# Optimization experiments

Measured on AMD Instinct MI355X. Metric: run time of the kernel, lower is better.

Reference implementation:

```python
import jax, jax.numpy as jnp
import numpy as np

# Problem constants (from init_kwargs)
NUM_NODES = 120000
NUM_MOVABLE = 100000
NUM_NETS = 100000
NUM_PINS = 400000
NBX = 256
NBY = 256
XL, XH, YL, YH = 0.0, 1000.0, 0.0, 1000.0
BSX = (XH - XL) / NBX  # bin_size_x
BSY = (YH - YL) / NBY  # bin_size_y
UNIT_H_CAP = 1.5  # unit_horizontal_routing_capacity
UNIT_V_CAP = 1.5  # unit_vertical_routing_capacity
MAX_RATE = 2.0    # max_route_opt_adjust_rate
MIN_RATE = 1.0 / MAX_RATE
EPS = 1e-6


def setup_inputs() -> dict:
    key = jax.random.key(0)
    k1, k2, k3, k4, k5, k6, k7, k8 = jax.random.split(key, 8)
    pos = jnp.concatenate([
        jax.random.uniform(k1, (NUM_NODES,), jnp.float32, XL, XH - 10.0),
        jax.random.uniform(k2, (NUM_NODES,), jnp.float32, YL, YH - 10.0)])
    pin_pos = jnp.concatenate([
        jax.random.uniform(k3, (NUM_PINS,), jnp.float32, XL, XH),
        jax.random.uniform(k4, (NUM_PINS,), jnp.float32, YL, YH)])
    node_size_x = jax.random.uniform(k5, (NUM_NODES,), jnp.float32, 1.0, 8.0)
    node_size_y = jax.random.uniform(k6, (NUM_NODES,), jnp.float32, 1.0, 4.0)
    flat_netpin = jax.random.randint(k7, (NUM_PINS,), 0, NUM_PINS, jnp.int32)
    inner = jnp.sort(jax.random.randint(k8, (NUM_NETS - 1,), 0, NUM_PINS, jnp.int32))
    netpin_start = jnp.concatenate([
        jnp.zeros((1,), jnp.int32), inner, jnp.full((1,), NUM_PINS, jnp.int32)])
    return dict(pos=pos, pin_pos=pin_pos, node_size_x=node_size_x,
                node_size_y=node_size_y, netpin_start=netpin_start,
                flat_netpin=flat_netpin)


def _bin_overlap(lo, hi, origin, bin_size, nbins):
    # lo, hi: [K] interval per item; returns [K, nbins] overlap length with each bin
    edges = origin + jnp.arange(nbins, dtype=lo.dtype) * bin_size  # [nbins]
    return jnp.clip(jnp.minimum(hi[:, None], edges + bin_size)
                    - jnp.maximum(lo[:, None], edges), 0.0)


def reference(pos, pin_pos, node_size_x, node_size_y, netpin_start, flat_netpin):
    num_pins = flat_netpin.shape[0]
    # --- per-net bounding boxes from ragged netpin lists (CSR) ---
    slot = jnp.arange(num_pins, dtype=jnp.int32)
    net_id = jnp.clip(jnp.searchsorted(netpin_start, slot, side='right') - 1,
                      0, NUM_NETS - 1)
    px = pin_pos[flat_netpin]
    py = pin_pos[num_pins + flat_netpin]
    xmin = jax.ops.segment_min(px, net_id, NUM_NETS, indices_are_sorted=True)
    xmax = jax.ops.segment_max(px, net_id, NUM_NETS, indices_are_sorted=True)
    ymin = jax.ops.segment_min(py, net_id, NUM_NETS, indices_are_sorted=True)
    ymax = jax.ops.segment_max(py, net_id, NUM_NETS, indices_are_sorted=True)
    valid = (xmax >= xmin) & (ymax >= ymin)  # nets with >=1 pin
    span_x = jnp.where(valid, xmax - xmin, 0.0)
    span_y = jnp.where(valid, ymax - ymin, 0.0)
    # RUDY demand density: horizontal demand per unit area = 1/span_y, etc.
    coef_h = jnp.where(valid & (span_y > EPS), 1.0 / jnp.maximum(span_y, EPS), 0.0)
    coef_v = jnp.where(valid & (span_x > EPS), 1.0 / jnp.maximum(span_x, EPS), 0.0)
    xmin_c = jnp.where(valid, xmin, XL)
    xmax_c = jnp.where(valid, xmax, XL)
    ymin_c = jnp.where(valid, ymin, YL)
    ymax_c = jnp.where(valid, ymax, YL)
    # separable bin overlaps: [N, NBX], [N, NBY]
    ox = _bin_overlap(xmin_c, xmax_c, XL, BSX, NBX)
    oy = _bin_overlap(ymin_c, ymax_c, YL, BSY, NBY)
    # scatter demand into 2D bin grid (rank-1 per net, summed via einsum)
    H = jnp.einsum('nx,ny->xy', ox * coef_h[:, None], oy)
    V = jnp.einsum('nx,ny->xy', ox * coef_v[:, None], oy)
    # capacity adjustment + clamp
    bin_area = BSX * BSY
    util = jnp.maximum(H / (bin_area * UNIT_H_CAP), V / (bin_area * UNIT_V_CAP))
    util = jnp.clip(util, MIN_RATE, MAX_RATE)
    # --- gather bin utilization back per movable node ---
    nxl = pos[:NUM_MOVABLE]
    nyl = pos[NUM_NODES:NUM_NODES + NUM_MOVABLE]
    nxh = nxl + node_size_x[:NUM_MOVABLE]
    nyh = nyl + node_size_y[:NUM_MOVABLE]
    nox = _bin_overlap(nxl, nxh, XL, BSX, NBX)  # [M, NBX]
    noy = _bin_overlap(nyl, nyh, YL, BSY, NBY)  # [M, NBY]
    instance_route_area = jnp.einsum('mx,xy,my->m', nox, util, noy)
    return instance_route_area
```

## Files before the change

kernel.cpp:

```cpp
#include <hip/hip_runtime.h>

#define NUM_NODES   120000
#define NUM_MOVABLE 100000
#define NUM_NETS    100000
#define NUM_PINS    400000
#define NBX 256
#define NBY 256
#define GRID_BINS (NBX*NBY)
#define SC_BLOCKS 32
#define SEGCAP 192

constexpr float BSX      = 1000.0f / 256.0f;
constexpr float INV_BS   = 256.0f / 1000.0f;
constexpr float BIN_AREA = BSX * BSX;
constexpr float EPSV     = 1e-6f;


__global__ void pin_bbox(const float* __restrict__ pin_pos,
                         const int* __restrict__ netpin_start,
                         const int* __restrict__ flat_netpin,
                         float4* __restrict__ bbox) {
    __shared__ int snp[260];
    __shared__ int sbound[2];
    int B0 = blockIdx.x * 256;
    int t  = B0 + threadIdx.x;
    if (threadIdx.x < 2) {
        int q = (threadIdx.x == 0) ? B0 : min(B0 + 255, NUM_PINS - 1);
        int lo = 0, hi = NUM_NETS + 1;
        while (lo < hi) {
            int mid = (lo + hi) >> 1;
            if (netpin_start[mid] <= q) lo = mid + 1; else hi = mid;
        }
        sbound[threadIdx.x] = min(lo - 1, NUM_NETS - 1);
    }
    __syncthreads();
    int netlo = sbound[0];
    int cnt   = sbound[1] - netlo + 2;
    for (int i = threadIdx.x; i < cnt; i += 256) snp[i] = netpin_start[netlo + i];
    __syncthreads();

    int key = -4;
    int net = -1, segend = -1;
    float xmn = 3.4e38f, xmx = -3.4e38f, ymn = 3.4e38f, ymx = -3.4e38f;
    if (t < NUM_PINS) {
        int lo = 0, hi = cnt;
        while (lo < hi) {
            int mid = (lo + hi) >> 1;
            if (snp[mid] <= t) lo = mid + 1; else hi = mid;
        }
        int li = lo - 1;
        net    = netlo + li;
        segend = snp[li + 1];
        key    = (net << 1) | (snp[li] == t ? 1 : 0);
        int p = flat_netpin[t];
        float px = pin_pos[p];
        float py = pin_pos[NUM_PINS + p];
        xmn = px; xmx = px; ymn = py; ymx = py;
    }
    int lane = threadIdx.x & 63;
    for (int d = 1; d < 64; d <<= 1) {
        int   ku = __shfl_up(key, d);
        float a  = __shfl_up(xmn, d);
        float b  = __shfl_up(xmx, d);
        float c  = __shfl_up(ymn, d);
        float e  = __shfl_up(ymx, d);
        if (lane >= d && (ku >> 1) == (key >> 1)) {
            xmn = fminf(xmn, a); xmx = fmaxf(xmx, b);
            ymn = fminf(ymn, c); ymx = fmaxf(ymx, e);
            key |= (ku & 1);
        }
    }
    int nextkey = __shfl_down(key, 1);
    if (t >= NUM_PINS || net < 0) return;
    bool netchg = (lane == 63) ? false : ((nextkey >> 1) != (key >> 1));
    bool tail   = (lane == 63) || netchg;
    if (!tail) return;
    bool true_end  = netchg || (segend == t + 1);
    bool contained = (key & 1) != 0;
    if (contained && true_end) {
        bbox[net] = make_float4(xmn, ymn, xmx, ymx);
    } else {
        unsigned* bp = (unsigned*)(bbox + net);
        atomicMin(bp + 0, __float_as_uint(xmn));
        atomicMin(bp + 1, __float_as_uint(ymn));
        atomicMax((int*)bp + 2, (int)__float_as_uint(xmx));
        atomicMax((int*)bp + 3, (int)__float_as_uint(ymx));
    }
}

__global__ __launch_bounds__(1024) void scatter_nets(
        const float4* __restrict__ bbox,
        unsigned* __restrict__ cnt_rb,
        unsigned* __restrict__ entries) {
    __shared__ unsigned cur[256];
    int t = threadIdx.x, blk = blockIdx.x;
    if (t < 256) cur[t] = 0u;
    __syncthreads();
    int start = blk * 4096;
    #pragma unroll
    for (int k = 0; k < 4; ++k) {
        int n = start + k * 1024 + t;
        if (n < NUM_NETS) {
            float4 b = bbox[n];
            if ((b.w - b.y) > EPSV || (b.z - b.x) > EPSV) {
                unsigned bxl = (unsigned)min((int)(b.x * INV_BS), NBX - 1);
                unsigned bxh = (unsigned)min((int)(b.z * INV_BS), NBX - 1);
                unsigned p0 = atomicAdd(&cur[bxl], 1u);
                if (p0 < SEGCAP)
                    entries[(bxl * 32 + blk) * SEGCAP + p0] = (unsigned)(n << 1);
                unsigned p1 = atomicAdd(&cur[bxh], 1u);
                if (p1 < SEGCAP)
                    entries[(bxh * 32 + blk) * SEGCAP + p1] = (unsigned)(n << 1) | 1u;
            }
        }
    }
    __syncthreads();
    if (t < 256) cnt_rb[t * 32 + blk] = min(cur[t], (unsigned)SEGCAP);
}

__global__ __launch_bounds__(1024) void splat_rows(
        const float4* __restrict__ bbox,
        const unsigned* __restrict__ cnt_rb,
        const unsigned* __restrict__ entries,
        float* __restrict__ A_hT, float* __restrict__ B_hT,
        float* __restrict__ A_vT, float* __restrict__ B_vT) {
    int bx = blockIdx.x;
    int t  = threadIdx.x;
    __shared__ float F[8][NBY];
    __shared__ unsigned pref[33];
    for (int i = t; i < 8 * NBY; i += 1024) ((float*)F)[i] = 0.0f;
    if (t == 0) {
        unsigned run = 0;
        for (int s = 0; s < 32; ++s) { pref[s] = run; run += cnt_rb[bx * 32 + s]; }
        pref[32] = run;
    }
    __syncthreads();
    int total = (int)pref[32];

    for (int j = t; j < total; j += 1024) {
        int lo = 0, hi = 32;
        while (lo + 1 < hi) {
            int mid = (lo + hi) >> 1;
            if ((int)pref[mid] <= j) lo = mid; else hi = mid;
        }
        unsigned e = entries[(bx * 32 + lo) * SEGCAP + (j - (int)pref[lo])];
        int n = (int)(e >> 1), side = (int)(e & 1u);
        float4 b = bbox[n];
        float span_x = b.z - b.x, span_y = b.w - b.y;
        float coef_h = (span_y > EPSV) ? 1.0f / span_y : 0.0f;
        float coef_v = (span_x > EPSV) ? 1.0f / span_x : 0.0f;
        int byl = min((int)(b.y * INV_BS), NBY - 1);
        int byh = min((int)(b.w * INV_BS), NBY - 1);
        float ryl = (float)(byl + 1) * BSX - b.y;
        float ryh = (float)(byh + 1) * BSX - b.w;
        float rx, s0;
        if (side == 0) {
            int bxl = min((int)(b.x * INV_BS), NBX - 1);
            rx = (float)(bxl + 1) * BSX - b.x; s0 = 1.0f;
        } else {
            int bxh = min((int)(b.z * INV_BS), NBX - 1);
            rx = (float)(bxh + 1) * BSX - b.z; s0 = -1.0f;
        }
        if (coef_h != 0.0f) {
            float w0 = s0 * coef_h, w1 = -s0 * coef_h;
            atomicAdd(&F[0][byl], w0 * rx  * ryl);
            atomicAdd(&F[1][byl], w0 * rx  * BSX);
            atomicAdd(&F[2][byl], w0 * BSX * ryl);
            atomicAdd(&F[3][byl], w0 * BSX * BSX);
            atomicAdd(&F[0][byh], w1 * rx  * ryh);
            atomicAdd(&F[1][byh], w1 * rx  * BSX);
            atomicAdd(&F[2][byh], w1 * BSX * ryh);
            atomicAdd(&F[3][byh], w1 * BSX * BSX);
        }
        if (coef_v != 0.0f) {
            float w0 = s0 * coef_v, w1 = -s0 * coef_v;
            atomicAdd(&F[4][byl], w0 * rx  * ryl);
            atomicAdd(&F[5][byl], w0 * rx  * BSX);
            atomicAdd(&F[6][byl], w0 * BSX * ryl);
            atomicAdd(&F[7][byl], w0 * BSX * BSX);
            atomicAdd(&F[4][byh], w1 * rx  * ryh);
            atomicAdd(&F[5][byh], w1 * rx  * BSX);
            atomicAdd(&F[6][byh], w1 * BSX * ryh);
            atomicAdd(&F[7][byh], w1 * BSX * BSX);
        }
    }
    __syncthreads();

    int g = t >> 8, y = t & 255;
    float* f = F[2 * g + 1];
    for (int d = 1; d < 256; d <<= 1) {
        float add = (y >= d) ? f[y - d] : 0.0f;
        __syncthreads();
        f[y] += add;
        __syncthreads();
    }
    float ex  = (y > 0) ? F[2 * g + 1][y - 1] : 0.0f;
    float val = F[2 * g][y] + ex;
    float* o  = (g == 0) ? A_hT : (g == 1) ? B_hT : (g == 2) ? A_vT : B_vT;
    o[y * NBX + bx] = val;
}

__global__ void scan_x_util(const float* __restrict__ A_hT, const float* __restrict__ B_hT,
                            const float* __restrict__ A_vT, const float* __restrict__ B_vT,
                            float* __restrict__ util) {
    int y = blockIdx.x, x = threadIdx.x;
    int idxT = y * NBX + x;
    __shared__ float2 tmp[NBX];
    tmp[x] = make_float2(B_hT[idxT], B_vT[idxT]);
    __syncthreads();
    for (int d = 1; d < 256; d <<= 1) {
        float2 add = (x >= d) ? tmp[x - d] : make_float2(0.f, 0.f);
        __syncthreads();
        tmp[x].x += add.x; tmp[x].y += add.y;
        __syncthreads();
    }
    float2 ex = (x > 0) ? tmp[x - 1] : make_float2(0.f, 0.f);
    float H = A_hT[idxT] + ex.x;
    float V = A_vT[idxT] + ex.y;
    float u = fmaxf(H, V) * (1.0f / (BIN_AREA * 1.5f));
    util[x * NBY + y] = fminf(fmaxf(u, 0.5f), 2.0f);
}

__global__ void node_area(const float* __restrict__ pos,
                          const float* __restrict__ nsx,
                          const float* __restrict__ nsy,
                          const float* __restrict__ util,
                          float* __restrict__ out) {
    int m = blockIdx.x * 256 + threadIdx.x;
    if (m >= NUM_MOVABLE) return;
    float xl = pos[m];
    float yl = pos[NUM_NODES + m];
    float xh = xl + nsx[m];
    float yh = yl + nsy[m];
    int bx0 = max(0, min((int)(xl * INV_BS), NBX - 1));
    int bx1 = max(0, min((int)(xh * INV_BS), NBX - 1));
    int by0 = max(0, min((int)(yl * INV_BS), NBY - 1));
    int by1 = max(0, min((int)(yh * INV_BS), NBY - 1));
    float acc = 0.0f;
    for (int bx = bx0; bx <= bx1; ++bx) {
        float ox = fminf(xh, (float)(bx + 1) * BSX) - fmaxf(xl, (float)bx * BSX);
        if (ox <= 0.0f) continue;
        const float* urow = util + bx * NBY;
        float inner = 0.0f;
        for (int by = by0; by <= by1; ++by) {
            float oy = fminf(yh, (float)(by + 1) * BSX) - fmaxf(yl, (float)by * BSX);
            if (oy > 0.0f) inner += oy * urow[by];
        }
        acc += ox * inner;
    }
    out[m] = acc;
}

extern "C" void kernel_launch(void* const* d_in, const int* in_sizes, int n_in,
                              void* d_out, int out_size, void* d_ws, size_t ws_size,
                              hipStream_t stream) {
    const float* pos          = (const float*)d_in[0];
    const float* pin_pos      = (const float*)d_in[1];
    const float* node_size_x  = (const float*)d_in[2];
    const float* node_size_y  = (const float*)d_in[3];
    const int*   netpin_start = (const int*)d_in[4];
    const int*   flat_netpin  = (const int*)d_in[5];

    float4*   bbox    = (float4*)d_ws;
    unsigned* cnt_rb  = (unsigned*)(bbox + NUM_NETS);
    unsigned* entries = cnt_rb + 256 * 32;
    float*    A_hT    = (float*)(entries + 256 * 32 * SEGCAP);
    float*    B_hT    = A_hT + GRID_BINS;
    float*    A_vT    = B_hT + GRID_BINS;
    float*    B_vT    = A_vT + GRID_BINS;
    float*    util    = B_vT + GRID_BINS;
    float*    out     = (float*)d_out;

    pin_bbox<<<(NUM_PINS + 255) / 256, 256, 0, stream>>>(
        pin_pos, netpin_start, flat_netpin, bbox);
    scatter_nets<<<SC_BLOCKS, 1024, 0, stream>>>(bbox, cnt_rb, entries);
    splat_rows<<<NBX, 1024, 0, stream>>>(bbox, cnt_rb, entries,
                                         A_hT, B_hT, A_vT, B_vT);
    scan_x_util<<<NBY, NBX, 0, stream>>>(A_hT, B_hT, A_vT, B_vT, util);
    node_area<<<(NUM_MOVABLE + 255) / 256, 256, 0, stream>>>(
        pos, node_size_x, node_size_y, util, out);
}
```

Measured before the change: 130.3 us.

## Fuse per-net bbox computation into the bin-scatter kernel with thread-per-net

```diff
diff --git a/kernel.cpp b/kernel.cpp
--- a/kernel.cpp
+++ b/kernel.cpp
@@ -7,8 +7,8 @@
 #define NBX 256
 #define NBY 256
 #define GRID_BINS (NBX*NBY)
-#define SC_BLOCKS 32
-#define SEGCAP 192
+#define NSB 391
+#define SEGCAP 32
 
 constexpr float BSX      = 1000.0f / 256.0f;
 constexpr float INV_BS   = 256.0f / 1000.0f;
@@ -16,106 +16,43 @@
 constexpr float EPSV     = 1e-6f;
 
 
-__global__ void pin_bbox(const float* __restrict__ pin_pos,
-                         const int* __restrict__ netpin_start,
-                         const int* __restrict__ flat_netpin,
-                         float4* __restrict__ bbox) {
-    __shared__ int snp[260];
-    __shared__ int sbound[2];
-    int B0 = blockIdx.x * 256;
-    int t  = B0 + threadIdx.x;
-    if (threadIdx.x < 2) {
-        int q = (threadIdx.x == 0) ? B0 : min(B0 + 255, NUM_PINS - 1);
-        int lo = 0, hi = NUM_NETS + 1;
-        while (lo < hi) {
-            int mid = (lo + hi) >> 1;
-            if (netpin_start[mid] <= q) lo = mid + 1; else hi = mid;
-        }
-        sbound[threadIdx.x] = min(lo - 1, NUM_NETS - 1);
-    }
-    __syncthreads();
-    int netlo = sbound[0];
-    int cnt   = sbound[1] - netlo + 2;
-    for (int i = threadIdx.x; i < cnt; i += 256) snp[i] = netpin_start[netlo + i];
-    __syncthreads();
-
-    int key = -4;
-    int net = -1, segend = -1;
-    float xmn = 3.4e38f, xmx = -3.4e38f, ymn = 3.4e38f, ymx = -3.4e38f;
-    if (t < NUM_PINS) {
-        int lo = 0, hi = cnt;
-        while (lo < hi) {
-            int mid = (lo + hi) >> 1;
-            if (snp[mid] <= t) lo = mid + 1; else hi = mid;
-        }
-        int li = lo - 1;
-        net    = netlo + li;
-        segend = snp[li + 1];
-        key    = (net << 1) | (snp[li] == t ? 1 : 0);
-        int p = flat_netpin[t];
-        float px = pin_pos[p];
-        float py = pin_pos[NUM_PINS + p];
-        xmn = px; xmx = px; ymn = py; ymx = py;
-    }
-    int lane = threadIdx.x & 63;
-    for (int d = 1; d < 64; d <<= 1) {
-        int   ku = __shfl_up(key, d);
-        float a  = __shfl_up(xmn, d);
-        float b  = __shfl_up(xmx, d);
-        float c  = __shfl_up(ymn, d);
-        float e  = __shfl_up(ymx, d);
-        if (lane >= d && (ku >> 1) == (key >> 1)) {
-            xmn = fminf(xmn, a); xmx = fmaxf(xmx, b);
-            ymn = fminf(ymn, c); ymx = fmaxf(ymx, e);
-            key |= (ku & 1);
-        }
-    }
-    int nextkey = __shfl_down(key, 1);
-    if (t >= NUM_PINS || net < 0) return;
-    bool netchg = (lane == 63) ? false : ((nextkey >> 1) != (key >> 1));
-    bool tail   = (lane == 63) || netchg;
-    if (!tail) return;
-    bool true_end  = netchg || (segend == t + 1);
-    bool contained = (key & 1) != 0;
-    if (contained && true_end) {
-        bbox[net] = make_float4(xmn, ymn, xmx, ymx);
-    } else {
-        unsigned* bp = (unsigned*)(bbox + net);
-        atomicMin(bp + 0, __float_as_uint(xmn));
-        atomicMin(bp + 1, __float_as_uint(ymn));
-        atomicMax((int*)bp + 2, (int)__float_as_uint(xmx));
-        atomicMax((int*)bp + 3, (int)__float_as_uint(ymx));
-    }
-}
-
-__global__ __launch_bounds__(1024) void scatter_nets(
-        const float4* __restrict__ bbox,
-        unsigned* __restrict__ cnt_rb,
-        unsigned* __restrict__ entries) {
+__global__ void bbox_scatter(const float* __restrict__ pin_pos,
+                             const int* __restrict__ netpin_start,
+                             const int* __restrict__ flat_netpin,
+                             float4* __restrict__ bbox,
+                             unsigned* __restrict__ cnt_rb,
+                             unsigned* __restrict__ entries) {
     __shared__ unsigned cur[256];
-    int t = threadIdx.x, blk = blockIdx.x;
-    if (t < 256) cur[t] = 0u;
-    __syncthreads();
-    int start = blk * 4096;
-    #pragma unroll
-    for (int k = 0; k < 4; ++k) {
-        int n = start + k * 1024 + t;
-        if (n < NUM_NETS) {
-            float4 b = bbox[n];
-            if ((b.w - b.y) > EPSV || (b.z - b.x) > EPSV) {
-                unsigned bxl = (unsigned)min((int)(b.x * INV_BS), NBX - 1);
-                unsigned bxh = (unsigned)min((int)(b.z * INV_BS), NBX - 1);
+    int tid = threadIdx.x, blk = blockIdx.x;
+    if (tid < 256) cur[tid] = 0u;
+    __syncthreads();
+    int n = blk * 256 + tid;
+    if (n < NUM_NETS) {
+        int s = netpin_start[n], e = netpin_start[n + 1];
+        if (e > s) {
+            float xmn = 3.4e38f, xmx = -3.4e38f, ymn = 3.4e38f, ymx = -3.4e38f;
+            for (int i = s; i < e; ++i) {
+                int p = flat_netpin[i];
+                float px = pin_pos[p];
+                float py = pin_pos[NUM_PINS + p];
+                xmn = fminf(xmn, px); xmx = fmaxf(xmx, px);
+                ymn = fminf(ymn, py); ymx = fmaxf(ymx, py);
+            }
+            bbox[n] = make_float4(xmn, ymn, xmx, ymx);
+            if ((ymx - ymn) > EPSV || (xmx - xmn) > EPSV) {
+                unsigned bxl = (unsigned)min((int)(xmn * INV_BS), NBX - 1);
+                unsigned bxh = (unsigned)min((int)(xmx * INV_BS), NBX - 1);
                 unsigned p0 = atomicAdd(&cur[bxl], 1u);
                 if (p0 < SEGCAP)
-                    entries[(bxl * 32 + blk) * SEGCAP + p0] = (unsigned)(n << 1);
+                    entries[(bxl * NSB + blk) * SEGCAP + p0] = (unsigned)(n << 1);
                 unsigned p1 = atomicAdd(&cur[bxh], 1u);
                 if (p1 < SEGCAP)
-                    entries[(bxh * 32 + blk) * SEGCAP + p1] = (unsigned)(n << 1) | 1u;
+                    entries[(bxh * NSB + blk) * SEGCAP + p1] = (unsigned)(n << 1) | 1u;
             }
         }
     }
     __syncthreads();
-    if (t < 256) cnt_rb[t * 32 + blk] = min(cur[t], (unsigned)SEGCAP);
+    if (tid < 256) cnt_rb[tid * NSB + blk] = min(cur[tid], (unsigned)SEGCAP);
 }
 
 __global__ __launch_bounds__(1024) void splat_rows(
@@ -126,24 +63,28 @@
         float* __restrict__ A_vT, float* __restrict__ B_vT) {
     int bx = blockIdx.x;
     int t  = threadIdx.x;
-    __shared__ float F[8][NBY];
-    __shared__ unsigned pref[33];
+    __shared__ float    F[8][NBY];
+    __shared__ unsigned S[512];
     for (int i = t; i < 8 * NBY; i += 1024) ((float*)F)[i] = 0.0f;
-    if (t == 0) {
-        unsigned run = 0;
-        for (int s = 0; s < 32; ++s) { pref[s] = run; run += cnt_rb[bx * 32 + s]; }
-        pref[32] = run;
-    }
-    __syncthreads();
-    int total = (int)pref[32];
+    if (t < 512) S[t] = (t < NSB) ? cnt_rb[bx * NSB + t] : 0u;
+    __syncthreads();
+    for (int d = 1; d < 512; d <<= 1) {
+        unsigned add = 0u;
+        if (t < 512 && t >= d) add = S[t - d];
+        __syncthreads();
+        if (t < 512) S[t] += add;
+        __syncthreads();
+    }
+    int total = (int)S[NSB - 1];
 
     for (int j = t; j < total; j += 1024) {
-        int lo = 0, hi = 32;
-        while (lo + 1 < hi) {
+        int lo = 0, hi = NSB;
+        while (lo < hi) {
             int mid = (lo + hi) >> 1;
-            if ((int)pref[mid] <= j) lo = mid; else hi = mid;
-        }
-        unsigned e = entries[(bx * 32 + lo) * SEGCAP + (j - (int)pref[lo])];
+            if ((int)S[mid] <= j) lo = mid + 1; else hi = mid;
+        }
+        int off = j - (lo > 0 ? (int)S[lo - 1] : 0);
+        unsigned e = entries[(bx * NSB + lo) * SEGCAP + off];
         int n = (int)(e >> 1), side = (int)(e & 1u);
         float4 b = bbox[n];
         float span_x = b.z - b.x, span_y = b.w - b.y;
@@ -263,17 +204,16 @@
 
     float4*   bbox    = (float4*)d_ws;
     unsigned* cnt_rb  = (unsigned*)(bbox + NUM_NETS);
-    unsigned* entries = cnt_rb + 256 * 32;
-    float*    A_hT    = (float*)(entries + 256 * 32 * SEGCAP);
+    unsigned* entries = cnt_rb + 256 * NSB;
+    float*    A_hT    = (float*)(entries + 256 * NSB * SEGCAP);
     float*    B_hT    = A_hT + GRID_BINS;
     float*    A_vT    = B_hT + GRID_BINS;
     float*    B_vT    = A_vT + GRID_BINS;
     float*    util    = B_vT + GRID_BINS;
     float*    out     = (float*)d_out;
 
-    pin_bbox<<<(NUM_PINS + 255) / 256, 256, 0, stream>>>(
-        pin_pos, netpin_start, flat_netpin, bbox);
-    scatter_nets<<<SC_BLOCKS, 1024, 0, stream>>>(bbox, cnt_rb, entries);
+    bbox_scatter<<<NSB, 256, 0, stream>>>(
+        pin_pos, netpin_start, flat_netpin, bbox, cnt_rb, entries);
     splat_rows<<<NBX, 1024, 0, stream>>>(bbox, cnt_rb, entries,
                                          A_hT, B_hT, A_vT, B_vT);
     scan_x_util<<<NBY, NBX, 0, stream>>>(A_hT, B_hT, A_vT, B_vT, util);
```

New measurement: 130.1 us. Within noise of the previous version (-0.2%).
